# Kernel optimization log

Hardware: AMD Instinct MI355X
Metric: run time of the kernel (lower is better)

## Reference

```python
import jax, jax.numpy as jnp
import numpy as np

D_MODEL = 1024
NUM_HEADS = 16
HEAD_DIM = D_MODEL // NUM_HEADS  # 64
MAX_SEQ_LEN = 2048
BASE = 10000.0


def _rope_tables(seq_len):
    # theta_i = base^(-2i/hd) for i in [0, hd/2)
    theta = 1.0 / (BASE ** (jnp.arange(0, HEAD_DIM, 2, dtype=jnp.float32) / HEAD_DIM))
    angles = jnp.arange(seq_len, dtype=jnp.float32)[:, None] * theta  # [S, hd/2]
    return jnp.cos(angles), jnp.sin(angles)


def _apply_rope(x, cos, sin):
    # x: [B, H, S, hd]; cos/sin: [S, hd/2] broadcast over B,H
    x1 = x[..., 0::2]
    x2 = x[..., 1::2]
    r1 = x1 * cos - x2 * sin
    r2 = x1 * sin + x2 * cos
    return jnp.stack([r1, r2], axis=-1).reshape(x.shape)  # interleave back


def setup_inputs() -> dict:
    key = jax.random.key(0)
    k_x, k_q, k_k, k_v, k_o = jax.random.split(key, 5)
    B, S = 2, 2048
    x = jax.random.normal(k_x, (B, S, D_MODEL), dtype=jnp.float32)
    init = 0.02
    w_q = jax.random.normal(k_q, (D_MODEL, D_MODEL), dtype=jnp.float32) * init
    w_k = jax.random.normal(k_k, (D_MODEL, D_MODEL), dtype=jnp.float32) * init
    w_v = jax.random.normal(k_v, (D_MODEL, D_MODEL), dtype=jnp.float32) * init
    w_o = jax.random.normal(k_o, (D_MODEL, D_MODEL), dtype=jnp.float32) * init
    return {"x": x, "w_q": w_q, "w_k": w_k, "w_v": w_v, "w_o": w_o}


def reference(x, w_q, w_k, w_v, w_o):
    # Prefill path: start_pos=0, cache=None, eval-mode dropout (identity).
    B, S, D = x.shape
    H, hd = NUM_HEADS, HEAD_DIM
    scale = 1.0 / (hd ** 0.5)

    # nn.Linear(bias=False): y = x @ W.T
    q = (x @ w_q.T).reshape(B, S, H, hd).transpose(0, 2, 1, 3)  # [B,H,S,hd]
    k = (x @ w_k.T).reshape(B, S, H, hd).transpose(0, 2, 1, 3)
    v = (x @ w_v.T).reshape(B, S, H, hd).transpose(0, 2, 1, 3)

    cos, sin = _rope_tables(S)  # same tables for every head (per-head torch loop vectorized)
    q_rot = _apply_rope(q, cos, sin)
    k_rot = _apply_rope(k, cos, sin)

    attn = jnp.einsum("bhqd,bhkd->bhqk", q_rot, k_rot) * scale  # [B,H,S,S]
    # causal mask: triu(ones(S,S), diagonal = S_k - S_q + 1 = 1)
    causal = jnp.triu(jnp.ones((S, S), dtype=bool), k=1)
    attn = jnp.where(causal[None, None], -jnp.inf, attn)
    attn_w = jax.nn.softmax(attn, axis=-1)

    out = jnp.einsum("bhqk,bhkd->bhqd", attn_w, v)  # [B,H,S,hd]
    out = out.transpose(0, 2, 1, 3).reshape(B, S, D)
    return out @ w_o.T
```

## Files before the change

kernel.cpp:

```cpp
#include <hip/hip_runtime.h>
#include <hip/hip_bf16.h>
#include <math.h>


#define S_LEN 2048
#define NHEADS 16
#define HD 64
#define DM 1024

typedef __attribute__((ext_vector_type(8))) short bf16x8;
typedef __attribute__((ext_vector_type(4))) float f32x4;

#define MFMA16(a, b, c) __builtin_amdgcn_mfma_f32_16x16x32_bf16((a), (b), (c), 0, 0, 0)
#define NEG_BIG (-1e30f)

#if __has_builtin(__builtin_amdgcn_exp2f)
#define EXP2F(x) __builtin_amdgcn_exp2f(x)
#else
#define EXP2F(x) exp2f(x)
#endif

#define GLOAD_LDS16(g, l)                                                      \
    __builtin_amdgcn_global_load_lds(                                          \
        (const __attribute__((address_space(1))) void*)(g),                    \
        (__attribute__((address_space(3))) void*)(l), 16, 0, 0)

__global__ __launch_bounds__(256) void convert_kernel(
    const float* __restrict__ x,  const float* __restrict__ wq,
    const float* __restrict__ wk, const float* __restrict__ wv,
    const float* __restrict__ wo,
    __hip_bfloat16* __restrict__ xb,  __hip_bfloat16* __restrict__ wqb,
    __hip_bfloat16* __restrict__ wkb, __hip_bfloat16* __restrict__ wvb,
    __hip_bfloat16* __restrict__ wob, float2* __restrict__ tab)
{
    const int y = blockIdx.y;
    if (y == 8) {
        const int gid = blockIdx.x * 256 + threadIdx.x;
        if (gid < S_LEN * 32) {
            const int s = gid >> 5, p = gid & 31;
            float theta = powf(10000.0f, -(float)(2 * p) * (1.0f / 64.0f));
            float sn, cs;
            sincosf((float)s * theta, &sn, &cs);
            tab[gid] = make_float2(cs, sn);
        }
        return;
    }
    const float* src;
    __hip_bfloat16* dst;
    size_t off = 0;
    if (y < 4)      { src = x;  dst = xb;  off = (size_t)y * 1048576; }
    else if (y == 4) { src = wq; dst = wqb; }
    else if (y == 5) { src = wk; dst = wkb; }
    else if (y == 6) { src = wv; dst = wvb; }
    else             { src = wo; dst = wob; }

    const size_t i = off + ((size_t)blockIdx.x * 256 + threadIdx.x) * 4;
    float4 v = *(const float4*)(src + i);
    __hip_bfloat16 t[4] = { __float2bfloat16(v.x), __float2bfloat16(v.y),
                            __float2bfloat16(v.z), __float2bfloat16(v.w) };
    *(ushort4*)(dst + i) = *(ushort4*)t;
}

__global__ __launch_bounds__(256) void qkv_kernel(
    const __hip_bfloat16* __restrict__ X,
    const __hip_bfloat16* __restrict__ Wq,
    const __hip_bfloat16* __restrict__ Wk,
    const __hip_bfloat16* __restrict__ Wv,
    __hip_bfloat16* __restrict__ qws,
    __hip_bfloat16* __restrict__ kws,
    __hip_bfloat16* __restrict__ vws)
{
    const int z = blockIdx.z;
    const bool vz = (z == 2);
    const __hip_bfloat16* __restrict__ Asrc = vz ? Wv : X;
    const __hip_bfloat16* __restrict__ Bsrc = vz ? X : ((z == 0) ? Wq : Wk);
    __hip_bfloat16* __restrict__ out = (z == 0) ? qws : (z == 1) ? kws : vws;

    __shared__ __align__(16) __hip_bfloat16 Asm[128 * 32];
    __shared__ __align__(16) __hip_bfloat16 Bsm[128 * 32];

    const int tid = threadIdx.x;
    const int wave = tid >> 6, lane = tid & 63;
    const int quad = lane >> 4, l15 = lane & 15;
    const int wm = (wave >> 1) * 64, wn = (wave & 1) * 64;
    const int m0 = vz ? blockIdx.x * 128 : blockIdx.y * 128;
    const int n0 = vz ? blockIdx.y * 128 : blockIdx.x * 128;

    f32x4 acc[4][4] = {};

    for (int k0 = 0; k0 < DM; k0 += 32) {
#pragma unroll
        for (int c = 0; c < 2; c++) {
            int idx = c * 2048 + tid * 8;
            int r = idx >> 5, kc = idx & 31;
            GLOAD_LDS16(Asrc + (size_t)(m0 + r) * DM + k0 + kc, &Asm[idx]);
            GLOAD_LDS16(Bsrc + (size_t)(n0 + r) * DM + k0 + kc, &Bsm[idx]);
        }
        __syncthreads();
        bf16x8 af[4], bfv[4];
#pragma unroll
        for (int i = 0; i < 4; i++)
            af[i] = *(const bf16x8*)(&Asm[(wm + i * 16 + l15) * 32 + quad * 8]);
#pragma unroll
        for (int j = 0; j < 4; j++)
            bfv[j] = *(const bf16x8*)(&Bsm[(wn + j * 16 + l15) * 32 + quad * 8]);
#pragma unroll
        for (int i = 0; i < 4; i++)
#pragma unroll
            for (int j = 0; j < 4; j++)
                acc[i][j] = MFMA16(af[i], bfv[j], acc[i][j]);
        __syncthreads();
    }

#pragma unroll
    for (int i = 0; i < 4; i++) {
#pragma unroll
        for (int r = 0; r < 4; r++) {
            int m = m0 + wm + i * 16 + quad * 4 + r;
#pragma unroll
            for (int j = 0; j < 4; j++) {
                int col = n0 + wn + j * 16 + l15;
                size_t idx;
                if (vz) {
                    int h = m >> 6, d = m & 63;
                    int b = col >> 11, s = col & 2047;
                    idx = (((size_t)(b * NHEADS + h)) * HD + d) * S_LEN + s;
                } else {
                    int b = m >> 11, s = m & 2047;
                    int h = col >> 6, d = col & 63;
                    idx = (((size_t)(b * NHEADS + h)) * S_LEN + s) * HD + d;
                }
                out[idx] = __float2bfloat16(acc[i][j][r]);
            }
        }
    }
}

__global__ __launch_bounds__(256) void rope_kernel(
    __hip_bfloat16* __restrict__ q, __hip_bfloat16* __restrict__ k,
    const float2* __restrict__ tab)
{
    __hip_bfloat16* __restrict__ p = (blockIdx.y == 0) ? q : k;
    const float qscale = (blockIdx.y == 0) ? 0.18033688011112042f
                                           : 1.0f;
    const int gid = blockIdx.x * 256 + threadIdx.x;
    const int e0 = gid * 8;
    const int s = (gid >> 3) & 2047;
    const int p4 = (gid & 7) * 4;

    const float2* tp = tab + s * 32 + p4;
    float4 t01 = *(const float4*)(tp);
    float4 t23 = *(const float4*)(tp + 2);
    float cs[4] = { t01.x, t01.z, t23.x, t23.z };
    float sn[4] = { t01.y, t01.w, t23.y, t23.w };

    int4 raw = *(const int4*)(p + e0);
    __hip_bfloat16* v = (__hip_bfloat16*)&raw;
#pragma unroll
    for (int i = 0; i < 4; i++) {
        float x1 = __bfloat162float(v[2 * i]);
        float x2 = __bfloat162float(v[2 * i + 1]);
        v[2 * i]     = __float2bfloat16((x1 * cs[i] - x2 * sn[i]) * qscale);
        v[2 * i + 1] = __float2bfloat16((x1 * sn[i] + x2 * cs[i]) * qscale);
    }
    *(int4*)(p + e0) = raw;
}


#define SM_STORE(sc, mm, ll, oo, Pr)                                           \
    do {                                                                       \
        float pm[4];                                                           \
        _Pragma("unroll")                                                      \
        for (int r = 0; r < 4; r++)                                            \
            pm[r] = fmaxf(fmaxf(sc[0][r], sc[1][r]),                           \
                          fmaxf(sc[2][r], sc[3][r]));                          \
        bool ok = true;                                                        \
        _Pragma("unroll")                                                      \
        for (int r = 0; r < 4; r++) ok = ok && (pm[r] <= mm[r] + 11.0f);       \
        if (!__all(ok)) {                                                      \
            _Pragma("unroll")                                                  \
            for (int off = 1; off < 16; off <<= 1)                             \
                _Pragma("unroll")                                              \
                for (int r = 0; r < 4; r++)                                    \
                    pm[r] = fmaxf(pm[r], __shfl_xor(pm[r], off));              \
            _Pragma("unroll")                                                  \
            for (int r = 0; r < 4; r++) {                                      \
                float mn = fmaxf(mm[r], pm[r]);                                \
                float al = EXP2F(mm[r] - mn);                                  \
                mm[r] = mn;                                                    \
                ll[r] *= al;                                                   \
                _Pragma("unroll")                                              \
                for (int t = 0; t < 4; t++) oo[t][r] *= al;                    \
            }                                                                  \
        }                                                                      \
        _Pragma("unroll")                                                      \
        for (int t = 0; t < 4; t++)                                            \
            _Pragma("unroll")                                                  \
            for (int r = 0; r < 4; r++)                                        \
                Pr[(quad * 4 + r) * 72 + t * 16 + l15] =                       \
                    __float2bfloat16(EXP2F(sc[t][r] - mm[r]));                 \
    } while (0)

#define PV_ACC(ll, oo, Pr)                                                     \
    do {                                                                       \
        _Pragma("unroll")                                                      \
        for (int st = 0; st < 2; st++) {                                       \
            bf16x8 pf = *(const bf16x8*)(&Pr[l15 * 72 + st * 32 + quad * 8]);  \
            __builtin_amdgcn_s_setprio(1);                                     \
            ll = MFMA16(pf, ones, ll);                                         \
            _Pragma("unroll")                                                  \
            for (int t = 0; t < 4; t++) oo[t] = MFMA16(pf, vf[st][t], oo[t]);  \
            __builtin_amdgcn_s_setprio(0);                                     \
        }                                                                      \
    } while (0)

#define LOAD_VF(kv0)                                                           \
    do {                                                                       \
        _Pragma("unroll")                                                      \
        for (int st = 0; st < 2; st++)                                         \
            _Pragma("unroll")                                                  \
            for (int t = 0; t < 4; t++)                                        \
                vf[st][t] = *(const bf16x8*)(Vtb +                             \
                    (size_t)(t * 16 + l15) * S_LEN + (kv0) + st * 32 + quad * 8); \
    } while (0)

#define LOAD_KF(kv0)                                                           \
    do {                                                                       \
        _Pragma("unroll")                                                      \
        for (int st = 0; st < 2; st++)                                         \
            _Pragma("unroll")                                                  \
            for (int t = 0; t < 4; t++)                                        \
                kf[st][t] = *(const bf16x8*)(Kb +                              \
                    (size_t)((kv0) + t * 16 + l15) * HD + st * 32 + quad * 8); \
    } while (0)

#define QK(sc, qf)                                                             \
    do {                                                                       \
        __builtin_amdgcn_s_setprio(1);                                         \
        _Pragma("unroll")                                                      \
        for (int st = 0; st < 2; st++)                                         \
            _Pragma("unroll")                                                  \
            for (int t = 0; t < 4; t++) sc[t] = MFMA16(qf[st], kf[st][t], sc[t]); \
        __builtin_amdgcn_s_setprio(0);                                         \
    } while (0)

#define MASK(sc, rowbase, kv0)                                                 \
    do {                                                                       \
        _Pragma("unroll")                                                      \
        for (int t = 0; t < 4; t++) {                                          \
            int col = (kv0) + t * 16 + l15;                                    \
            _Pragma("unroll")                                                  \
            for (int r = 0; r < 4; r++) {                                      \
                int row = (rowbase) + quad * 4 + r;                            \
                if (col > row) sc[t][r] = NEG_BIG;                             \
            }                                                                  \
        }                                                                      \
    } while (0)

__global__ __launch_bounds__(256) void attn_kernel(
    const __hip_bfloat16* __restrict__ Qg,
    const __hip_bfloat16* __restrict__ Kg,
    const __hip_bfloat16* __restrict__ Vtg,
    __hip_bfloat16* __restrict__ Og)
{
    const int bh = blockIdx.x;
    const int qi = (blockIdx.y < 8) ? blockIdx.y : 23 - blockIdx.y;
    const int tid = threadIdx.x;
    const int w = tid >> 6, lane = tid & 63;
    const int quad = lane >> 4, l15 = lane & 15;
    const size_t base = (size_t)bh * S_LEN * HD;
    const __hip_bfloat16* Qb = Qg + base;
    const __hip_bfloat16* Kb = Kg + base;
    const __hip_bfloat16* Vtb = Vtg + base;
    const int b = bh >> 4, h = bh & 15;

    __shared__ __align__(16) __hip_bfloat16 Pl[128 * 72];
    __hip_bfloat16* PrA = &Pl[w * 32 * 72];
    __hip_bfloat16* PrB = PrA + 16 * 72;

    const int q0 = qi * 128;
    const int rowA = q0 + w * 16;
    const int rowB = rowA + 64;

    bf16x8 qfA[2], qfB[2];
#pragma unroll
    for (int st = 0; st < 2; st++) {
        qfA[st] = *(const bf16x8*)(Qb + (size_t)(rowA + l15) * HD + st * 32 + quad * 8);
        qfB[st] = *(const bf16x8*)(Qb + (size_t)(rowB + l15) * HD + st * 32 + quad * 8);
    }

    bf16x8 ones;
#pragma unroll
    for (int i = 0; i < 8; i++) ones[i] = (short)0x3F80;

    float mA[4], mB[4];
    f32x4 lA = {}, lB = {};
    f32x4 oA[4] = {}, oB[4] = {};
#pragma unroll
    for (int r = 0; r < 4; r++) { mA[r] = NEG_BIG; mB[r] = NEG_BIG; }

    bf16x8 kf[2][4];
    bf16x8 vf[2][4];

    LOAD_KF(0);
    f32x4 scA[4] = {}, scB[4] = {};
    QK(scA, qfA);
    QK(scB, qfB);
    LOAD_KF(64);

#pragma unroll 1
    for (int j = 0; j < 2 * qi; j++) {
        const int kv0 = j * 64;
        LOAD_VF(kv0);
        f32x4 scAn[4] = {}, scBn[4] = {};
        QK(scAn, qfA);
        QK(scBn, qfB);
        LOAD_KF(kv0 + 128);
        SM_STORE(scA, mA, lA, oA, PrA);
        SM_STORE(scB, mB, lB, oB, PrB);
        PV_ACC(lA, oA, PrA);
        PV_ACC(lB, oB, PrB);
#pragma unroll
        for (int t = 0; t < 4; t++) { scA[t] = scAn[t]; scB[t] = scBn[t]; }
    }

    {
        const int kv0 = q0;
        LOAD_VF(kv0);
        f32x4 scBn[4] = {};
        QK(scBn, qfB);
        MASK(scA, rowA, kv0);
        SM_STORE(scA, mA, lA, oA, PrA);
        SM_STORE(scB, mB, lB, oB, PrB);
        PV_ACC(lA, oA, PrA);
        PV_ACC(lB, oB, PrB);

        const int kv1 = kv0 + 64;
        LOAD_VF(kv1);
        MASK(scBn, rowB, kv1);
        SM_STORE(scBn, mB, lB, oB, PrB);
        PV_ACC(lB, oB, PrB);
    }

#pragma unroll
    for (int t = 0; t < 4; t++)
#pragma unroll
        for (int r = 0; r < 4; r++) {
            int d = t * 16 + l15;
            int sA = rowA + quad * 4 + r;
            Og[((size_t)(b * S_LEN + sA)) * DM + h * HD + d] =
                __float2bfloat16(oA[t][r] / lA[r]);
            int sB = rowB + quad * 4 + r;
            Og[((size_t)(b * S_LEN + sB)) * DM + h * HD + d] =
                __float2bfloat16(oB[t][r] / lB[r]);
        }
}

__global__ __launch_bounds__(256) void oproj_kernel(
    const __hip_bfloat16* __restrict__ A,
    const __hip_bfloat16* __restrict__ W,
    float* __restrict__ out)
{
    __shared__ __align__(16) __hip_bfloat16 Asm[128 * 32];
    __shared__ __align__(16) __hip_bfloat16 Bsm[128 * 32];

    const int tid = threadIdx.x;
    const int wave = tid >> 6, lane = tid & 63;
    const int quad = lane >> 4, l15 = lane & 15;
    const int wm = (wave >> 1) * 64, wn = (wave & 1) * 64;
    const int m0 = blockIdx.y * 128, n0 = blockIdx.x * 128;

    f32x4 acc[4][4] = {};

    for (int k0 = 0; k0 < DM; k0 += 32) {
#pragma unroll
        for (int c = 0; c < 2; c++) {
            int idx = c * 2048 + tid * 8;
            int r = idx >> 5, kc = idx & 31;
            GLOAD_LDS16(A + (size_t)(m0 + r) * DM + k0 + kc, &Asm[idx]);
            GLOAD_LDS16(W + (size_t)(n0 + r) * DM + k0 + kc, &Bsm[idx]);
        }
        __syncthreads();
        bf16x8 af[4], bfv[4];
#pragma unroll
        for (int i = 0; i < 4; i++)
            af[i] = *(const bf16x8*)(&Asm[(wm + i * 16 + l15) * 32 + quad * 8]);
#pragma unroll
        for (int j = 0; j < 4; j++)
            bfv[j] = *(const bf16x8*)(&Bsm[(wn + j * 16 + l15) * 32 + quad * 8]);
#pragma unroll
        for (int i = 0; i < 4; i++)
#pragma unroll
            for (int j = 0; j < 4; j++)
                acc[i][j] = MFMA16(af[i], bfv[j], acc[i][j]);
        __syncthreads();
    }

#pragma unroll
    for (int i = 0; i < 4; i++)
#pragma unroll
        for (int r = 0; r < 4; r++) {
            int m = m0 + wm + i * 16 + quad * 4 + r;
#pragma unroll
            for (int j = 0; j < 4; j++) {
                int col = n0 + wn + j * 16 + l15;
                __hip_bfloat16 bb = __float2bfloat16(acc[i][j][r]);
                unsigned int u = ((unsigned int)(*(unsigned short*)&bb)) << 16;
                out[(size_t)m * DM + col] = __uint_as_float(u);
            }
        }
}

extern "C" void kernel_launch(void* const* d_in, const int* in_sizes, int n_in,
                              void* d_out, int out_size, void* d_ws, size_t ws_size,
                              hipStream_t stream)
{
    const float* x  = (const float*)d_in[0];
    const float* wq = (const float*)d_in[1];
    const float* wk = (const float*)d_in[2];
    const float* wv = (const float*)d_in[3];
    const float* wo = (const float*)d_in[4];
    float* out = (float*)d_out;

    const size_t xe = (size_t)2 * S_LEN * DM;
    const size_t we = (size_t)DM * DM;
    __hip_bfloat16* xb  = (__hip_bfloat16*)d_ws;
    __hip_bfloat16* wqb = xb + xe;
    __hip_bfloat16* wkb = wqb + we;
    __hip_bfloat16* wvb = wkb + we;
    __hip_bfloat16* wob = wvb + we;
    __hip_bfloat16* qws = wob + we;
    __hip_bfloat16* kws = qws + xe;
    __hip_bfloat16* vws = kws + xe;
    __hip_bfloat16* aws = vws + xe;
    float2* tab = (float2*)aws;

    dim3 blk(256, 1, 1);
    convert_kernel<<<dim3(1024, 9, 1), blk, 0, stream>>>(x, wq, wk, wv, wo,
                                                         xb, wqb, wkb, wvb, wob, tab);
    qkv_kernel<<<dim3(8, 32, 3), blk, 0, stream>>>(xb, wqb, wkb, wvb, qws, kws, vws);
    rope_kernel<<<dim3(2048, 2, 1), blk, 0, stream>>>(qws, kws, tab);
    attn_kernel<<<dim3(32, 16, 1), blk, 0, stream>>>(qws, kws, vws, aws);
    oproj_kernel<<<dim3(8, 32, 1), blk, 0, stream>>>(aws, wob, out);
}
```

Before: 212.4 us.

## Fuse RoPE into QKV GEMM epilogue via per-head weight row permutation

Permutes Q and K weight rows during bf16 conversion so each head's even and odd dims become contiguous halves. The QKV GEMM epilogue can then apply the rotation and the q scale in registers before storing, and the separate rope kernel is removed. This saves a launch and a full read-modify-write pass over q and k. It relies on q and k sharing the same permuted head-dim layout, which leaves attention scores unchanged, and it adds table loads to the GEMM epilogue.

```diff
diff --git a/kernel.cpp b/kernel.cpp
--- a/kernel.cpp
+++ b/kernel.cpp
@@ -48,9 +48,10 @@
     const float* src;
     __hip_bfloat16* dst;
     size_t off = 0;
+    bool perm = false;
     if (y < 4)      { src = x;  dst = xb;  off = (size_t)y * 1048576; }
-    else if (y == 4) { src = wq; dst = wqb; }
-    else if (y == 5) { src = wk; dst = wkb; }
+    else if (y == 4) { src = wq; dst = wqb; perm = true; }
+    else if (y == 5) { src = wk; dst = wkb; perm = true; }
     else if (y == 6) { src = wv; dst = wvb; }
     else             { src = wo; dst = wob; }
 
@@ -58,7 +59,14 @@
     float4 v = *(const float4*)(src + i);
     __hip_bfloat16 t[4] = { __float2bfloat16(v.x), __float2bfloat16(v.y),
                             __float2bfloat16(v.z), __float2bfloat16(v.w) };
-    *(ushort4*)(dst + i) = *(ushort4*)t;
+    size_t o = i;
+    if (perm) {
+        int row = (int)(i >> 10), colk = (int)(i & 1023);
+        int hh = row >> 6, dd = row & 63;
+        int dstore = (dd & 1) ? (32 + (dd >> 1)) : (dd >> 1);
+        o = (((size_t)((hh << 6) + dstore)) << 10) + colk;
+    }
+    *(ushort4*)(dst + o) = *(ushort4*)t;
 }
 
 __global__ __launch_bounds__(256) void qkv_kernel(
@@ -68,13 +76,16 @@
     const __hip_bfloat16* __restrict__ Wv,
     __hip_bfloat16* __restrict__ qws,
     __hip_bfloat16* __restrict__ kws,
-    __hip_bfloat16* __restrict__ vws)
+    __hip_bfloat16* __restrict__ vws,
+    const float2* __restrict__ tab)
 {
     const int z = blockIdx.z;
     const bool vz = (z == 2);
     const __hip_bfloat16* __restrict__ Asrc = vz ? Wv : X;
     const __hip_bfloat16* __restrict__ Bsrc = vz ? X : ((z == 0) ? Wq : Wk);
     __hip_bfloat16* __restrict__ out = (z == 0) ? qws : (z == 1) ? kws : vws;
+    const float qscale = (z == 0) ? 0.18033688011112042f
+                                  : 1.0f;
 
     __shared__ __align__(16) __hip_bfloat16 Asm[128 * 32];
     __shared__ __align__(16) __hip_bfloat16 Bsm[128 * 32];
@@ -110,6 +121,25 @@
             for (int j = 0; j < 4; j++)
                 acc[i][j] = MFMA16(af[i], bfv[j], acc[i][j]);
         __syncthreads();
+    }
+
+    if (!vz) {
+#pragma unroll
+        for (int i = 0; i < 4; i++)
+#pragma unroll
+            for (int r = 0; r < 4; r++) {
+                int m = m0 + wm + i * 16 + quad * 4 + r;
+                int s = m & 2047;
+#pragma unroll
+                for (int j = 0; j < 2; j++) {
+                    int p = j * 16 + l15;
+                    float2 t = tab[s * 32 + p];
+                    float x1 = acc[i][j][r];
+                    float x2 = acc[i][j + 2][r];
+                    acc[i][j][r]     = (x1 * t.x - x2 * t.y) * qscale;
+                    acc[i][j + 2][r] = (x1 * t.y + x2 * t.x) * qscale;
+                }
+            }
     }
 
 #pragma unroll
@@ -134,36 +164,6 @@
             }
         }
     }
-}
-
-__global__ __launch_bounds__(256) void rope_kernel(
-    __hip_bfloat16* __restrict__ q, __hip_bfloat16* __restrict__ k,
-    const float2* __restrict__ tab)
-{
-    __hip_bfloat16* __restrict__ p = (blockIdx.y == 0) ? q : k;
-    const float qscale = (blockIdx.y == 0) ? 0.18033688011112042f
-                                           : 1.0f;
-    const int gid = blockIdx.x * 256 + threadIdx.x;
-    const int e0 = gid * 8;
-    const int s = (gid >> 3) & 2047;
-    const int p4 = (gid & 7) * 4;
-
-    const float2* tp = tab + s * 32 + p4;
-    float4 t01 = *(const float4*)(tp);
-    float4 t23 = *(const float4*)(tp + 2);
-    float cs[4] = { t01.x, t01.z, t23.x, t23.z };
-    float sn[4] = { t01.y, t01.w, t23.y, t23.w };
-
-    int4 raw = *(const int4*)(p + e0);
-    __hip_bfloat16* v = (__hip_bfloat16*)&raw;
-#pragma unroll
-    for (int i = 0; i < 4; i++) {
-        float x1 = __bfloat162float(v[2 * i]);
-        float x2 = __bfloat162float(v[2 * i + 1]);
-        v[2 * i]     = __float2bfloat16((x1 * cs[i] - x2 * sn[i]) * qscale);
-        v[2 * i + 1] = __float2bfloat16((x1 * sn[i] + x2 * cs[i]) * qscale);
-    }
-    *(int4*)(p + e0) = raw;
 }
 
 
@@ -438,8 +438,8 @@
     dim3 blk(256, 1, 1);
     convert_kernel<<<dim3(1024, 9, 1), blk, 0, stream>>>(x, wq, wk, wv, wo,
                                                          xb, wqb, wkb, wvb, wob, tab);
-    qkv_kernel<<<dim3(8, 32, 3), blk, 0, stream>>>(xb, wqb, wkb, wvb, qws, kws, vws);
-    rope_kernel<<<dim3(2048, 2, 1), blk, 0, stream>>>(qws, kws, tab);
+    qkv_kernel<<<dim3(8, 32, 3), blk, 0, stream>>>(xb, wqb, wkb, wvb,
+                                                   qws, kws, vws, tab);
     attn_kernel<<<dim3(32, 16, 1), blk, 0, stream>>>(qws, kws, vws, aws);
     oproj_kernel<<<dim3(8, 32, 1), blk, 0, stream>>>(aws, wob, out);
 }
```

New measurement: 223.9 us. +5.4%, slower.
